# Kernel tuning notes

Measured on AMD Instinct MI355X. Metric: run time of the kernel, lower is better.

The kernel has to match this reference:

```python
import jax, jax.numpy as jnp
import numpy as np

D_IN = 1024
D_OUT = 1024
NUM_HEADS = 16
HEAD_DIM = D_OUT // NUM_HEADS
EPS = 1e-6
POW = 16.0


def setup_inputs() -> dict:
    key = jax.random.key(0)
    ks = jax.random.split(key, 6)
    s = 1.0 / np.sqrt(D_IN)
    x = jax.random.normal(ks[0], (2, 2048, D_IN), dtype=jnp.float32)
    Wq = jax.random.uniform(ks[1], (D_OUT, D_IN), jnp.float32, -s, s)
    Wk = jax.random.uniform(ks[2], (D_OUT, D_IN), jnp.float32, -s, s)
    Wv = jax.random.uniform(ks[3], (D_OUT, D_IN), jnp.float32, -s, s)
    Wo = jax.random.uniform(ks[4], (D_OUT, D_OUT), jnp.float32, -s, s)
    bo = jax.random.uniform(ks[5], (D_OUT,), jnp.float32, -s, s)
    return {"x": x, "Wq": Wq, "Wk": Wk, "Wv": Wv, "Wo": Wo, "bo": bo}


def _l2norm(t):
    # torch F.normalize: t / max(||t||, eps)
    n = jnp.sqrt(jnp.sum(t * t, axis=-1, keepdims=True))
    return t / jnp.maximum(n, EPS)


def reference(x, Wq, Wk, Wv, Wo, bo):
    B, T, _ = x.shape
    # project and split heads: [B, H, T, Dh]
    def heads(W):
        y = jnp.einsum('btd,od->bto', x, W)
        return y.reshape(B, T, NUM_HEADS, HEAD_DIM).transpose(0, 2, 1, 3)
    Q = _l2norm(heads(Wq))
    K = _l2norm(heads(Wk))
    V = heads(Wv)
    cos_sim = jnp.clip(jnp.einsum('bhtd,bhsd->bhts', Q, K), -0.999, 0.999)
    scores = 1.0 - jnp.arccos(cos_sim) / jnp.pi
    W = jnp.power(jnp.maximum(scores, EPS), POW)
    W = W / (jnp.sum(W, axis=-1, keepdims=True) + EPS)
    out = jnp.einsum('bhts,bhsd->bhtd', W, V)
    out = out.transpose(0, 2, 1, 3).reshape(B, T, D_OUT)
    return jnp.einsum('bto,po->btp', out, Wo) + bo
```

## Files before the change

### kernel.cpp

```cpp
#include <hip/hip_runtime.h>
#include <math.h>

constexpr int Dm   = 1024;
constexpr int NH   = 16;
constexpr int HD   = 64;
constexpr int Bb   = 2;
constexpr int Tt   = 2048;
constexpr int MTOT = Bb * Tt;
#define EPSF 1e-6f

typedef __attribute__((ext_vector_type(8))) short short8;
typedef __attribute__((ext_vector_type(4))) float f32x4;
typedef __attribute__((ext_vector_type(2))) float f32x2;

__device__ __forceinline__ ushort f2bf(float f) {
    union { float f; unsigned u; } v; v.f = f;
    unsigned r = (v.u + 0x7FFFu + ((v.u >> 16) & 1u)) >> 16;
    return (ushort)r;
}

__device__ __forceinline__ unsigned cvt_pk_bf16(float lo, float hi) {
    unsigned r;
    asm("v_cvt_pk_bf16_f32 %0, %1, %2" : "=v"(r) : "v"(lo), "v"(hi));
    return r;
}

__device__ __forceinline__ void gload16(const void* g, void* l) {
    __builtin_amdgcn_global_load_lds(
        (const __attribute__((address_space(1))) unsigned int*)g,
        (__attribute__((address_space(3))) unsigned int*)l,
        16, 0, 0);
}

__global__ __launch_bounds__(256)
void cvt_all(const float* __restrict__ x,  const float* __restrict__ wq,
             const float* __restrict__ wk, const float* __restrict__ wv,
             const float* __restrict__ wo,
             ushort* __restrict__ xb,  ushort* __restrict__ wqb,
             ushort* __restrict__ wkb, ushort* __restrict__ wvb,
             ushort* __restrict__ wob) {
    int i = blockIdx.x * 256 + threadIdx.x;
    const float* src; ushort* dst; int off;
    if (i < 1048576)      { src = x;  dst = xb;  off = i; }
    else if (i < 1310720) { src = wq; dst = wqb; off = i - 1048576; }
    else if (i < 1572864) { src = wk; dst = wkb; off = i - 1310720; }
    else if (i < 1835008) { src = wv; dst = wvb; off = i - 1572864; }
    else                  { src = wo; dst = wob; off = i - 1835008; }
    const float4 v = ((const float4*)src)[off];
    ushort4 o;
    o.x = f2bf(v.x); o.y = f2bf(v.y); o.z = f2bf(v.z); o.w = f2bf(v.w);
    ((ushort4*)dst)[off] = o;
}

template<bool OUTF32>
__device__ __forceinline__
void gemm_core(const ushort* __restrict__ A, const ushort* __restrict__ W,
               const float* __restrict__ bias, void* __restrict__ out,
               int m0, int n0, int N, int K, int mode) {
    __shared__ ushort As[128 * 64];
    __shared__ ushort Bs[128 * 64];
    const int tid  = threadIdx.x;
    const int wave = tid >> 6, lane = tid & 63;
    const int quad = lane >> 4, l15 = lane & 15;
    const int wr = wave >> 1, wc = wave & 1;
    const int lr = lane >> 3;
    const int sc = (lane & 7) ^ lr;

    f32x4 acc[4][4] = {};
    const ushort* Ab = A + (size_t)(m0 + lr) * K + sc * 8;
    const ushort* Wb = W + (size_t)(n0 + lr) * K + sc * 8;

    for (int k0 = 0; k0 < K; k0 += 64) {
        #pragma unroll
        for (int i = 0; i < 4; i++) {
            const int rows8 = (wave * 4 + i) * 8;
            gload16(Ab + (size_t)rows8 * K + k0, &As[rows8 * 64]);
            gload16(Wb + (size_t)rows8 * K + k0, &Bs[rows8 * 64]);
        }
        __syncthreads();
        #pragma unroll
        for (int kh = 0; kh < 2; kh++) {
            short8 af[4];
            #pragma unroll
            for (int mi = 0; mi < 4; mi++) {
                const int row = wr * 64 + mi * 16 + l15;
                af[mi] = *(const short8*)&As[row * 64 + (((kh * 4 + quad) ^ (row & 7)) * 8)];
            }
            #pragma unroll
            for (int nj = 0; nj < 4; nj++) {
                const int row = wc * 64 + nj * 16 + l15;
                const short8 bf = *(const short8*)&Bs[row * 64 + (((kh * 4 + quad) ^ (row & 7)) * 8)];
                #pragma unroll
                for (int mi = 0; mi < 4; mi++)
                    acc[mi][nj] = __builtin_amdgcn_mfma_f32_16x16x32_bf16(af[mi], bf, acc[mi][nj], 0, 0, 0);
            }
        }
        __syncthreads();
    }

    if (!OUTF32 && mode == 2) {
        #pragma unroll
        for (int mi = 0; mi < 4; mi++) {
            const int t  = m0 + wr * 64 + mi * 16 + quad * 4;
            const int bb = t >> 11, tl = t & 2047;
            #pragma unroll
            for (int nj = 0; nj < 4; nj++) {
                const int n = n0 + wc * 64 + nj * 16 + l15;
                const int hh = n >> 6, dd = n & 63;
                uint2 pk;
                pk.x = (unsigned)f2bf(acc[mi][nj][0]) | ((unsigned)f2bf(acc[mi][nj][1]) << 16);
                pk.y = (unsigned)f2bf(acc[mi][nj][2]) | ((unsigned)f2bf(acc[mi][nj][3]) << 16);
                *(uint2*)&((ushort*)out)[(size_t)((bb * NH + hh) * HD + dd) * Tt + tl] = pk;
            }
        }
        return;
    }

    #pragma unroll
    for (int mi = 0; mi < 4; mi++) {
        float inv[4] = {1.f, 1.f, 1.f, 1.f};
        if (!OUTF32 && mode == 1) {
            #pragma unroll
            for (int r = 0; r < 4; r++) {
                float ss = 0.f;
                #pragma unroll
                for (int nj = 0; nj < 4; nj++) ss += acc[mi][nj][r] * acc[mi][nj][r];
                ss += __shfl_xor(ss, 1); ss += __shfl_xor(ss, 2);
                ss += __shfl_xor(ss, 4); ss += __shfl_xor(ss, 8);
                inv[r] = 1.f / fmaxf(sqrtf(ss), EPSF);
            }
        }
        #pragma unroll
        for (int nj = 0; nj < 4; nj++)
            #pragma unroll
            for (int r = 0; r < 4; r++) {
                const int row = m0 + wr * 64 + mi * 16 + quad * 4 + r;
                const int col = n0 + wc * 64 + nj * 16 + l15;
                if (OUTF32)
                    ((float*)out)[(size_t)row * N + col] = acc[mi][nj][r] + bias[col];
                else
                    ((ushort*)out)[(size_t)row * N + col] = f2bf(acc[mi][nj][r] * inv[r]);
            }
    }
}

__global__ __launch_bounds__(256)
void qkv_gemm(const ushort* __restrict__ xb,
              const ushort* __restrict__ wq, const ushort* __restrict__ wk,
              const ushort* __restrict__ wv,
              ushort* __restrict__ qb, ushort* __restrict__ kb,
              ushort* __restrict__ vtb) {
    const int ny = blockIdx.y, sel = ny >> 3;
    const ushort* W = (sel == 0) ? wq : (sel == 1) ? wk : wv;
    ushort* out     = (sel == 0) ? qb : (sel == 1) ? kb : vtb;
    gemm_core<false>(xb, W, nullptr, out, blockIdx.x * 128, (ny & 7) * 128,
                     Dm, Dm, (sel < 2) ? 1 : 2);
}

__global__ __launch_bounds__(256)
void out_gemm(const ushort* __restrict__ A, const ushort* __restrict__ W,
              const float* __restrict__ bias, float* __restrict__ out) {
    __shared__ ushort As[64 * 64];
    __shared__ ushort Bs[128 * 64];
    const int tid  = threadIdx.x;
    const int wave = tid >> 6, lane = tid & 63;
    const int quad = lane >> 4, l15 = lane & 15;
    const int wm = wave & 1, wn = wave >> 1;
    const int lr = lane >> 3;
    const int sc = (lane & 7) ^ lr;
    const int m0 = blockIdx.x * 64, n0 = blockIdx.y * 128;
    const int K = Dm, N = Dm;

    f32x4 acc[2][4] = {};
    const ushort* Ab = A + (size_t)(m0 + lr) * K + sc * 8;
    const ushort* Wb = W + (size_t)(n0 + lr) * K + sc * 8;

    for (int k0 = 0; k0 < K; k0 += 64) {
        #pragma unroll
        for (int i = 0; i < 2; i++) {
            const int rows8 = (wave * 2 + i) * 8;
            gload16(Ab + (size_t)rows8 * K + k0, &As[rows8 * 64]);
        }
        #pragma unroll
        for (int i = 0; i < 4; i++) {
            const int rows8 = (wave * 4 + i) * 8;
            gload16(Wb + (size_t)rows8 * K + k0, &Bs[rows8 * 64]);
        }
        __syncthreads();
        #pragma unroll
        for (int kh = 0; kh < 2; kh++) {
            short8 af[2];
            #pragma unroll
            for (int mi = 0; mi < 2; mi++) {
                const int row = wm * 32 + mi * 16 + l15;
                af[mi] = *(const short8*)&As[row * 64 + (((kh * 4 + quad) ^ (row & 7)) * 8)];
            }
            #pragma unroll
            for (int nj = 0; nj < 4; nj++) {
                const int row = wn * 64 + nj * 16 + l15;
                const short8 bf = *(const short8*)&Bs[row * 64 + (((kh * 4 + quad) ^ (row & 7)) * 8)];
                #pragma unroll
                for (int mi = 0; mi < 2; mi++)
                    acc[mi][nj] = __builtin_amdgcn_mfma_f32_16x16x32_bf16(af[mi], bf, acc[mi][nj], 0, 0, 0);
            }
        }
        __syncthreads();
    }
    #pragma unroll
    for (int mi = 0; mi < 2; mi++)
        #pragma unroll
        for (int nj = 0; nj < 4; nj++)
            #pragma unroll
            for (int r = 0; r < 4; r++) {
                const int row = m0 + wm * 32 + mi * 16 + quad * 4 + r;
                const int col = n0 + wn * 64 + nj * 16 + l15;
                out[(size_t)row * N + col] = acc[mi][nj][r] + bias[col];
            }
}

__global__ __launch_bounds__(512, 8)
void attn_kernel(const ushort* __restrict__ Qb, const ushort* __restrict__ Kb,
                 const ushort* __restrict__ Vtb, ushort* __restrict__ Ob) {
    __shared__ char smem[32768 + 256];
    const int tid  = threadIdx.x;
    const int wave = tid >> 6, lane = tid & 63;
    const int team = wave >> 2, wq = wave & 3;
    const int quad = lane >> 4, l15 = lane & 15;
    const int t0 = blockIdx.x * 64, h = blockIdx.y, b = blockIdx.z;
    const int tb = team << 14;

    const size_t qrow = (size_t)(b * Tt + t0 + 16 * wq + l15) * Dm + h * HD;
    const short8 qf0 = *(const short8*)&Qb[qrow + quad * 8];
    const short8 qf1 = *(const short8*)&Qb[qrow + 32 + quad * 8];

    const int tt   = tid & 255;
    const int r0k  = tt >> 3, ch0k = tt & 7;
    const int r0v  = tt >> 2, ch0v = tt & 3;
    const int lswK = r0k * 64 + ((ch0k ^ (r0k & 7)) * 8);
    const int lswV = r0v * 32 + ((ch0v ^ (r0v & 3)) * 8);

    const size_t kbase  = (size_t)(b * Tt) * Dm + h * HD;
    const size_t vtbase = (size_t)((b * NH + h) * HD) * Tt;
    const ushort* kg = Kb  + kbase  + (size_t)(team * 1024 + r0k) * Dm + ch0k * 8;
    const ushort* vg = Vtb + vtbase + (size_t)r0v * Tt + team * 1024 + ch0v * 8;

    f32x4 oacc[4] = {};
    f32x2 denp = {0.f, 0.f};

    const f32x2 h3 = { 0.011180f,  0.011180f};
    const f32x2 h2 = {-0.002070f, -0.002070f};
    const f32x2 h1 = { 0.040732f,  0.040732f};
    const f32x2 h0 = { 0.450158f,  0.450158f};

    short8 pk0 = *(const short8*)kg;
    short8 pv0 = *(const short8*)vg;
    *(short8*)((char*)smem + tb + lswK * 2) = pk0;
    *(short8*)((char*)smem + tb + 8192 + lswV * 2) = pv0;
    __syncthreads();

    const ushort* kgp = kg + (size_t)32 * Dm;
    const ushort* vgp = vg + 32;

    for (int i = 0; i < 32; i++) {
        const int p = i & 1;
        const ushort* Kp = (const ushort*)(smem + tb + (p << 12));
        const ushort* Vp = (const ushort*)(smem + tb + 8192 + (p << 12));
        if (i < 31) {
            pk0 = *(const short8*)kgp;
            pv0 = *(const short8*)vgp;
            kgp += (size_t)32 * Dm;
            vgp += 32;
        }

        f32x4 sfT[2] = {};
        #pragma unroll
        for (int j = 0; j < 2; j++) {
            const int row = 16 * j + l15;
            const short8 kf0 = *(const short8*)&Kp[row * 64 + ((quad ^ (row & 7)) * 8)];
            const short8 kf1 = *(const short8*)&Kp[row * 64 + (((4 + quad) ^ (row & 7)) * 8)];
            sfT[j] = __builtin_amdgcn_mfma_f32_16x16x32_bf16(kf0, qf0, sfT[j], 0, 0, 0);
            sfT[j] = __builtin_amdgcn_mfma_f32_16x16x32_bf16(kf1, qf1, sfT[j], 0, 0, 0);
        }

        f32x2 wA[4];
        #pragma unroll
        for (int r = 0; r < 4; r++) {
            f32x2 tA;
            tA.x = __builtin_amdgcn_fmed3f(1.0f - sfT[0][r], 0.001f, 1.999f);
            tA.y = __builtin_amdgcn_fmed3f(1.0f - sfT[1][r], 0.001f, 1.999f);
            f32x2 pa = __builtin_elementwise_fma(tA, h3, h2);
            pa = __builtin_elementwise_fma(pa, tA, h1);
            pa = __builtin_elementwise_fma(pa, tA, h0);
            f32x2 ra;
            ra.x = __builtin_amdgcn_sqrtf(tA.x); ra.y = __builtin_amdgcn_sqrtf(tA.y);
            const f32x2 one2 = {1.0f, 1.0f};
            f32x2 wa = __builtin_elementwise_fma(-ra, pa, one2);
            wa *= wa; wa *= wa; wa *= wa; wa *= wa;
            denp += wa;
            wA[r] = wa;
        }

        unsigned L0 = cvt_pk_bf16(wA[0].x, wA[1].x);
        unsigned L1 = cvt_pk_bf16(wA[0].y, wA[1].y);
        unsigned H0 = cvt_pk_bf16(wA[2].x, wA[3].x);
        unsigned H1 = cvt_pk_bf16(wA[2].y, wA[3].y);
        asm("v_permlane32_swap_b32 %0, %1" : "+v"(L0), "+v"(L1));
        asm("v_permlane16_swap_b32 %0, %1" : "+v"(L0), "+v"(L1));
        asm("v_permlane32_swap_b32 %0, %1" : "+v"(H0), "+v"(H1));
        asm("v_permlane16_swap_b32 %0, %1" : "+v"(H0), "+v"(H1));
        int4 bi1; bi1.x = (int)L0; bi1.y = (int)H0; bi1.z = (int)L1; bi1.w = (int)H1;
        const short8 Bf1 = __builtin_bit_cast(short8, bi1);

        #pragma unroll
        for (int jd = 0; jd < 4; jd++) {
            const int vrow = 16 * jd + l15;
            const short8 vf = *(const short8*)&Vp[vrow * 32 + ((quad ^ (vrow & 3)) * 8)];
            oacc[jd] = __builtin_amdgcn_mfma_f32_16x16x32_bf16(vf, Bf1, oacc[jd], 0, 0, 0);
        }

        if (i < 31) {
            *(short8*)((char*)smem + tb + ((1 - p) << 12) + lswK * 2) = pk0;
            *(short8*)((char*)smem + tb + 8192 + ((1 - p) << 12) + lswV * 2) = pv0;
        }
        __syncthreads();
    }

    float d = denp.x + denp.y;
    d += __shfl_xor(d, 16);
    d += __shfl_xor(d, 32);

    float* Obuf = (float*)smem;
    float* Den  = (float*)(smem + 32768);
    const int q = 16 * wq + l15;

    if (team == 1) {
        #pragma unroll
        for (int jd = 0; jd < 4; jd++)
            #pragma unroll
            for (int r = 0; r < 4; r++)
                Obuf[q * 64 + 16 * jd + quad * 4 + r] = oacc[jd][r];
        if (quad == 0) Den[q] = d;
    }
    __syncthreads();

    if (team == 0) {
        const float inv = __builtin_amdgcn_rcpf(d + Den[q] + EPSF);
        const size_t orow = (size_t)(b * Tt + t0 + q) * Dm + h * HD;
        #pragma unroll
        for (int jd = 0; jd < 4; jd++) {
            float o0 = (oacc[jd][0] + Obuf[q * 64 + 16 * jd + quad * 4 + 0]) * inv;
            float o1 = (oacc[jd][1] + Obuf[q * 64 + 16 * jd + quad * 4 + 1]) * inv;
            float o2 = (oacc[jd][2] + Obuf[q * 64 + 16 * jd + quad * 4 + 2]) * inv;
            float o3 = (oacc[jd][3] + Obuf[q * 64 + 16 * jd + quad * 4 + 3]) * inv;
            uint2 pk2;
            pk2.x = cvt_pk_bf16(o0, o1);
            pk2.y = cvt_pk_bf16(o2, o3);
            *(uint2*)&Ob[orow + 16 * jd + quad * 4] = pk2;
        }
    }
}

extern "C" void kernel_launch(void* const* d_in, const int* in_sizes, int n_in,
                              void* d_out, int out_size, void* d_ws, size_t ws_size,
                              hipStream_t stream) {
    const float* x  = (const float*)d_in[0];
    const float* Wq = (const float*)d_in[1];
    const float* Wk = (const float*)d_in[2];
    const float* Wv = (const float*)d_in[3];
    const float* Wo = (const float*)d_in[4];
    const float* bo = (const float*)d_in[5];
    float* out = (float*)d_out;

    ushort* ws = (ushort*)d_ws;
    const size_t M1 = 1u << 20;
    ushort* xb  = ws;
    ushort* wqb = ws + 4 * M1;
    ushort* wkb = ws + 5 * M1;
    ushort* wvb = ws + 6 * M1;
    ushort* wob = ws + 7 * M1;
    ushort* qb  = ws + 8 * M1;
    ushort* kb  = ws + 12 * M1;
    ushort* vtb = ws + 16 * M1;
    ushort* aob = ws + 20 * M1;

    cvt_all<<<8192, 256, 0, stream>>>(x, Wq, Wk, Wv, Wo, xb, wqb, wkb, wvb, wob);
    qkv_gemm<<<dim3(MTOT / 128, 24), 256, 0, stream>>>(xb, wqb, wkb, wvb, qb, kb, vtb);
    attn_kernel<<<dim3(Tt / 64, NH, Bb), 512, 0, stream>>>(qb, kb, vtb, aob);
    out_gemm<<<dim3(MTOT / 64, Dm / 128), 256, 0, stream>>>(aob, wob, bo, out);
}
```

Before: 224.2 us.

## Switch attention kernel to 32x32x16 MFMA tiles with 4-wave blocks

Rewrites the attention inner loop to use 32x32x16 bf16 MFMA instead of 16x16x32, with each wave covering 32 queries instead of 16 and blocks shrunk from 8 to 4 waves (two key-splitting teams of two waves). The LDS layout for K and V tiles changes, with V rows padded instead of swizzled, and the permlane shuffle that builds the P operand is simplified. The aim is fewer MFMA and LDS-read instructions per score element and more reuse of K/V fragments. In exchange each lane holds more accumulator registers, and per-CU occupancy changes.

```diff
diff --git a/kernel.cpp b/kernel.cpp
--- a/kernel.cpp
+++ b/kernel.cpp
@@ -11,6 +11,7 @@
 
 typedef __attribute__((ext_vector_type(8))) short short8;
 typedef __attribute__((ext_vector_type(4))) float f32x4;
+typedef __attribute__((ext_vector_type(16))) float f32x16;
 typedef __attribute__((ext_vector_type(2))) float f32x2;
 
 __device__ __forceinline__ ushort f2bf(float f) {
@@ -218,33 +219,36 @@
             }
 }
 
-__global__ __launch_bounds__(512, 8)
+__global__ __launch_bounds__(256, 4)
 void attn_kernel(const ushort* __restrict__ Qb, const ushort* __restrict__ Kb,
                  const ushort* __restrict__ Vtb, ushort* __restrict__ Ob) {
-    __shared__ char smem[32768 + 256];
+    __shared__ __attribute__((aligned(16))) char smem[37120];
     const int tid  = threadIdx.x;
     const int wave = tid >> 6, lane = tid & 63;
-    const int team = wave >> 2, wq = wave & 3;
-    const int quad = lane >> 4, l15 = lane & 15;
+    const int s = wave & 1, tm = wave >> 1;
+    const int l31 = lane & 31, H = lane >> 5;
     const int t0 = blockIdx.x * 64, h = blockIdx.y, b = blockIdx.z;
-    const int tb = team << 14;
-
-    const size_t qrow = (size_t)(b * Tt + t0 + 16 * wq + l15) * Dm + h * HD;
-    const short8 qf0 = *(const short8*)&Qb[qrow + quad * 8];
-    const short8 qf1 = *(const short8*)&Qb[qrow + 32 + quad * 8];
-
-    const int tt   = tid & 255;
-    const int r0k  = tt >> 3, ch0k = tt & 7;
-    const int r0v  = tt >> 2, ch0v = tt & 3;
-    const int lswK = r0k * 64 + ((ch0k ^ (r0k & 7)) * 8);
-    const int lswV = r0v * 32 + ((ch0v ^ (r0v & 3)) * 8);
-
+    char* tbase = smem + tm * 18432;
+
+    const size_t qrow = (size_t)(b * Tt + t0 + 32 * s + l31) * Dm + h * HD;
+    short8 qf[4];
+    #pragma unroll
+    for (int c = 0; c < 4; c++)
+        qf[c] = *(const short8*)&Qb[qrow + 16 * c + 8 * H];
+
+    const int tt = tid & 127;
+    const int rk = tt >> 2, ck = (tt & 3) * 2;
+    const int rv = tt >> 1, cv = (tt & 1) * 2;
     const size_t kbase  = (size_t)(b * Tt) * Dm + h * HD;
     const size_t vtbase = (size_t)((b * NH + h) * HD) * Tt;
-    const ushort* kg = Kb  + kbase  + (size_t)(team * 1024 + r0k) * Dm + ch0k * 8;
-    const ushort* vg = Vtb + vtbase + (size_t)r0v * Tt + team * 1024 + ch0v * 8;
-
-    f32x4 oacc[4] = {};
+    const ushort* kg = Kb  + kbase  + (size_t)(tm * 1024 + rk) * Dm + ck * 8;
+    const ushort* vg = Vtb + vtbase + (size_t)rv * Tt + tm * 1024 + cv * 8;
+    const int kw0 = rk * 128 + ((ck ^ (rk & 7)) * 16);
+    const int kw1 = rk * 128 + (((ck + 1) ^ (rk & 7)) * 16);
+    const int vw0 = rv * 80 + cv * 16;
+    const int vw1 = vw0 + 16;
+
+    f32x16 oacc[2] = {};
     f32x2 denp = {0.f, 0.f};
 
     const f32x2 h3 = { 0.011180f,  0.011180f};
@@ -253,9 +257,13 @@
     const f32x2 h0 = { 0.450158f,  0.450158f};
 
     short8 pk0 = *(const short8*)kg;
+    short8 pk1 = *(const short8*)(kg + 8);
     short8 pv0 = *(const short8*)vg;
-    *(short8*)((char*)smem + tb + lswK * 2) = pk0;
-    *(short8*)((char*)smem + tb + 8192 + lswV * 2) = pv0;
+    short8 pv1 = *(const short8*)(vg + 8);
+    *(short8*)(tbase + kw0) = pk0;
+    *(short8*)(tbase + kw1) = pk1;
+    *(short8*)(tbase + 4096 + vw0) = pv0;
+    *(short8*)(tbase + 4096 + vw1) = pv1;
     __syncthreads();
 
     const ushort* kgp = kg + (size_t)32 * Dm;
@@ -263,31 +271,30 @@
 
     for (int i = 0; i < 32; i++) {
         const int p = i & 1;
-        const ushort* Kp = (const ushort*)(smem + tb + (p << 12));
-        const ushort* Vp = (const ushort*)(smem + tb + 8192 + (p << 12));
+        const ushort* Kp = (const ushort*)(tbase + p * 9216);
+        const ushort* Vp = (const ushort*)(tbase + p * 9216 + 4096);
         if (i < 31) {
             pk0 = *(const short8*)kgp;
+            pk1 = *(const short8*)(kgp + 8);
             pv0 = *(const short8*)vgp;
+            pv1 = *(const short8*)(vgp + 8);
             kgp += (size_t)32 * Dm;
             vgp += 32;
         }
 
-        f32x4 sfT[2] = {};
-        #pragma unroll
-        for (int j = 0; j < 2; j++) {
-            const int row = 16 * j + l15;
-            const short8 kf0 = *(const short8*)&Kp[row * 64 + ((quad ^ (row & 7)) * 8)];
-            const short8 kf1 = *(const short8*)&Kp[row * 64 + (((4 + quad) ^ (row & 7)) * 8)];
-            sfT[j] = __builtin_amdgcn_mfma_f32_16x16x32_bf16(kf0, qf0, sfT[j], 0, 0, 0);
-            sfT[j] = __builtin_amdgcn_mfma_f32_16x16x32_bf16(kf1, qf1, sfT[j], 0, 0, 0);
-        }
-
-        f32x2 wA[4];
-        #pragma unroll
-        for (int r = 0; r < 4; r++) {
+        f32x16 sf = {};
+        #pragma unroll
+        for (int c = 0; c < 4; c++) {
+            const short8 kf = *(const short8*)&Kp[l31 * 64 + (((2 * c + H) ^ (l31 & 7)) * 8)];
+            sf = __builtin_amdgcn_mfma_f32_32x32x16_bf16(kf, qf[c], sf, 0, 0, 0);
+        }
+
+        f32x2 w2[8];
+        #pragma unroll
+        for (int ii = 0; ii < 8; ii++) {
             f32x2 tA;
-            tA.x = __builtin_amdgcn_fmed3f(1.0f - sfT[0][r], 0.001f, 1.999f);
-            tA.y = __builtin_amdgcn_fmed3f(1.0f - sfT[1][r], 0.001f, 1.999f);
+            tA.x = __builtin_amdgcn_fmed3f(1.0f - sf[2 * ii],     0.001f, 1.999f);
+            tA.y = __builtin_amdgcn_fmed3f(1.0f - sf[2 * ii + 1], 0.001f, 1.999f);
             f32x2 pa = __builtin_elementwise_fma(tA, h3, h2);
             pa = __builtin_elementwise_fma(pa, tA, h1);
             pa = __builtin_elementwise_fma(pa, tA, h0);
@@ -297,66 +304,81 @@
             f32x2 wa = __builtin_elementwise_fma(-ra, pa, one2);
             wa *= wa; wa *= wa; wa *= wa; wa *= wa;
             denp += wa;
-            wA[r] = wa;
-        }
-
-        unsigned L0 = cvt_pk_bf16(wA[0].x, wA[1].x);
-        unsigned L1 = cvt_pk_bf16(wA[0].y, wA[1].y);
-        unsigned H0 = cvt_pk_bf16(wA[2].x, wA[3].x);
-        unsigned H1 = cvt_pk_bf16(wA[2].y, wA[3].y);
-        asm("v_permlane32_swap_b32 %0, %1" : "+v"(L0), "+v"(L1));
-        asm("v_permlane16_swap_b32 %0, %1" : "+v"(L0), "+v"(L1));
-        asm("v_permlane32_swap_b32 %0, %1" : "+v"(H0), "+v"(H1));
-        asm("v_permlane16_swap_b32 %0, %1" : "+v"(H0), "+v"(H1));
-        int4 bi1; bi1.x = (int)L0; bi1.y = (int)H0; bi1.z = (int)L1; bi1.w = (int)H1;
-        const short8 Bf1 = __builtin_bit_cast(short8, bi1);
-
-        #pragma unroll
-        for (int jd = 0; jd < 4; jd++) {
-            const int vrow = 16 * jd + l15;
-            const short8 vf = *(const short8*)&Vp[vrow * 32 + ((quad ^ (vrow & 3)) * 8)];
-            oacc[jd] = __builtin_amdgcn_mfma_f32_16x16x32_bf16(vf, Bf1, oacc[jd], 0, 0, 0);
+            w2[ii] = wa;
+        }
+
+        unsigned P0 = cvt_pk_bf16(w2[0].x, w2[0].y);
+        unsigned P1 = cvt_pk_bf16(w2[1].x, w2[1].y);
+        unsigned P2 = cvt_pk_bf16(w2[2].x, w2[2].y);
+        unsigned P3 = cvt_pk_bf16(w2[3].x, w2[3].y);
+        unsigned P4 = cvt_pk_bf16(w2[4].x, w2[4].y);
+        unsigned P5 = cvt_pk_bf16(w2[5].x, w2[5].y);
+        unsigned P6 = cvt_pk_bf16(w2[6].x, w2[6].y);
+        unsigned P7 = cvt_pk_bf16(w2[7].x, w2[7].y);
+        asm("v_permlane32_swap_b32 %0, %1" : "+v"(P0), "+v"(P2));
+        asm("v_permlane32_swap_b32 %0, %1" : "+v"(P1), "+v"(P3));
+        asm("v_permlane32_swap_b32 %0, %1" : "+v"(P4), "+v"(P6));
+        asm("v_permlane32_swap_b32 %0, %1" : "+v"(P5), "+v"(P7));
+        int4 bi0; bi0.x = (int)P0; bi0.y = (int)P1; bi0.z = (int)P2; bi0.w = (int)P3;
+        int4 bi1; bi1.x = (int)P4; bi1.y = (int)P5; bi1.z = (int)P6; bi1.w = (int)P7;
+        const short8 B0 = __builtin_bit_cast(short8, bi0);
+        const short8 B1 = __builtin_bit_cast(short8, bi1);
+
+        #pragma unroll
+        for (int dd = 0; dd < 2; dd++) {
+            const int vr = 32 * dd + l31;
+            const short8 vf0 = *(const short8*)&Vp[vr * 40 + H * 8];
+            const short8 vf1 = *(const short8*)&Vp[vr * 40 + (2 + H) * 8];
+            oacc[dd] = __builtin_amdgcn_mfma_f32_32x32x16_bf16(vf0, B0, oacc[dd], 0, 0, 0);
+            oacc[dd] = __builtin_amdgcn_mfma_f32_32x32x16_bf16(vf1, B1, oacc[dd], 0, 0, 0);
         }
 
         if (i < 31) {
-            *(short8*)((char*)smem + tb + ((1 - p) << 12) + lswK * 2) = pk0;
-            *(short8*)((char*)smem + tb + 8192 + ((1 - p) << 12) + lswV * 2) = pv0;
+            char* nb = tbase + (1 - p) * 9216;
+            *(short8*)(nb + kw0) = pk0;
+            *(short8*)(nb + kw1) = pk1;
+            *(short8*)(nb + 4096 + vw0) = pv0;
+            *(short8*)(nb + 4096 + vw1) = pv1;
         }
         __syncthreads();
     }
 
     float d = denp.x + denp.y;
-    d += __shfl_xor(d, 16);
     d += __shfl_xor(d, 32);
 
     float* Obuf = (float*)smem;
-    float* Den  = (float*)(smem + 32768);
-    const int q = 16 * wq + l15;
-
-    if (team == 1) {
-        #pragma unroll
-        for (int jd = 0; jd < 4; jd++)
-            #pragma unroll
-            for (int r = 0; r < 4; r++)
-                Obuf[q * 64 + 16 * jd + quad * 4 + r] = oacc[jd][r];
-        if (quad == 0) Den[q] = d;
+    float* Den  = (float*)(smem + 36864);
+    const int ql = 32 * s + l31;
+
+    if (tm == 1) {
+        #pragma unroll
+        for (int dd = 0; dd < 2; dd++)
+            #pragma unroll
+            for (int rg = 0; rg < 16; rg++) {
+                const int dloc = 32 * dd + (rg & 3) + 8 * (rg >> 2) + 4 * H;
+                Obuf[ql * 64 + dloc] = oacc[dd][rg];
+            }
+        if (H == 0) Den[ql] = d;
     }
     __syncthreads();
 
-    if (team == 0) {
-        const float inv = __builtin_amdgcn_rcpf(d + Den[q] + EPSF);
-        const size_t orow = (size_t)(b * Tt + t0 + q) * Dm + h * HD;
-        #pragma unroll
-        for (int jd = 0; jd < 4; jd++) {
-            float o0 = (oacc[jd][0] + Obuf[q * 64 + 16 * jd + quad * 4 + 0]) * inv;
-            float o1 = (oacc[jd][1] + Obuf[q * 64 + 16 * jd + quad * 4 + 1]) * inv;
-            float o2 = (oacc[jd][2] + Obuf[q * 64 + 16 * jd + quad * 4 + 2]) * inv;
-            float o3 = (oacc[jd][3] + Obuf[q * 64 + 16 * jd + quad * 4 + 3]) * inv;
-            uint2 pk2;
-            pk2.x = cvt_pk_bf16(o0, o1);
-            pk2.y = cvt_pk_bf16(o2, o3);
-            *(uint2*)&Ob[orow + 16 * jd + quad * 4] = pk2;
-        }
+    if (tm == 0) {
+        const float inv = __builtin_amdgcn_rcpf(d + Den[ql] + EPSF);
+        const size_t orow = (size_t)(b * Tt + t0 + ql) * Dm + h * HD;
+        #pragma unroll
+        for (int dd = 0; dd < 2; dd++)
+            #pragma unroll
+            for (int g = 0; g < 4; g++) {
+                const int dbase = 32 * dd + 8 * g + 4 * H;
+                const float o0 = (oacc[dd][4 * g + 0] + Obuf[ql * 64 + dbase + 0]) * inv;
+                const float o1 = (oacc[dd][4 * g + 1] + Obuf[ql * 64 + dbase + 1]) * inv;
+                const float o2 = (oacc[dd][4 * g + 2] + Obuf[ql * 64 + dbase + 2]) * inv;
+                const float o3 = (oacc[dd][4 * g + 3] + Obuf[ql * 64 + dbase + 3]) * inv;
+                uint2 pk2;
+                pk2.x = cvt_pk_bf16(o0, o1);
+                pk2.y = cvt_pk_bf16(o2, o3);
+                *(uint2*)&Ob[orow + dbase] = pk2;
+            }
     }
 }
 
@@ -385,6 +407,6 @@
 
     cvt_all<<<8192, 256, 0, stream>>>(x, Wq, Wk, Wv, Wo, xb, wqb, wkb, wvb, wob);
     qkv_gemm<<<dim3(MTOT / 128, 24), 256, 0, stream>>>(xb, wqb, wkb, wvb, qb, kb, vtb);
-    attn_kernel<<<dim3(Tt / 64, NH, Bb), 512, 0, stream>>>(qb, kb, vtb, aob);
+    attn_kernel<<<dim3(Tt / 64, NH, Bb), 256, 0, stream>>>(qb, kb, vtb, aob);
     out_gemm<<<dim3(MTOT / 64, Dm / 128), 256, 0, stream>>>(aob, wob, bo, out);
 }
```

Result: faster. 214.9 us (-4.2%).
